# Kernel tuning notes

Hardware: AMD Instinct MI355X
Metric: run time of the kernel (lower is better)

The kernel has to match this reference:

```python
import jax, jax.numpy as jnp
import numpy as np

KEEP_P = 0.75  # 1 - dropout_p, dropout_p = 0.25

def setup_inputs() -> dict:
    key = jax.random.key(0)
    k1, k2, k3, k4 = jax.random.split(key, 4)
    B, Sq, Skv, D, Dv = 8, 2048, 2048, 128, 128
    x1 = jax.random.normal(k1, (B, Sq, D), dtype=jnp.float32)
    x2 = jax.random.normal(k2, (B, Skv, D), dtype=jnp.float32)
    x3 = jax.random.normal(k3, (B, Skv, Dv), dtype=jnp.float32)
    # torch Dropout(p): mask = bernoulli(keep_p) / keep_p
    keep = jax.random.bernoulli(k4, KEEP_P, (B, Sq, Skv))
    dropout_mask = keep.astype(jnp.float32) / KEEP_P
    return {"x1": x1, "x2": x2, "x3": x3, "dropout_mask": dropout_mask}

def reference(x1, x2, x3, dropout_mask):
    # scores: [B, Sq, Skv] = x1 @ x2^T (no scale: scale_factor is None)
    scores = jnp.einsum("bqd,bkd->bqk", x1, x2)
    probs = jax.nn.softmax(scores, axis=-1)
    probs = probs * dropout_mask  # dropout with fixed mask
    out = jnp.einsum("bqk,bkv->bqv", probs, x3)  # [B, Sq, Dv]
    return out
```

## Files before the change

### kernel.cpp

```cpp
#include <hip/hip_runtime.h>
#include <stdint.h>

#define SQ 2048
#define SKV 2048
#define DD 128
#define NB 8
#define LOG2E 1.44269504088896340736f
#define M0L 57.70780163555852f

typedef float    f4v __attribute__((ext_vector_type(4)));
typedef __bf16   bf8 __attribute__((ext_vector_type(8)));
typedef _Float16 h8  __attribute__((ext_vector_type(8)));

__device__ __forceinline__ void async16(const void* g, void* l) {
    __builtin_amdgcn_global_load_lds(
        (const __attribute__((address_space(1))) void*)g,
        (__attribute__((address_space(3))) void*)l, 16, 0, 0);
}

__global__ void preprocess(const float* __restrict__ x2, _Float16* __restrict__ Kh,
                           const float* __restrict__ x3, __bf16* __restrict__ VTf) {
    __shared__ __bf16 tile[32][33];
    const int bid = blockIdx.x;
    if (bid < 1024) {
        int tid = bid * 256 + threadIdx.x;
        int d8 = tid & 15;
        int kv = (tid >> 4) & (SKV - 1);
        int b  = tid >> 15;
        const float* p = x2 + ((size_t)b * SKV + kv) * DD + d8 * 8;
        f4v a0 = *(const f4v*)p;
        f4v a1 = *(const f4v*)(p + 4);
        h8 h;
#pragma unroll
        for (int c = 0; c < 4; c++) {
            h[c]     = (_Float16)a0[c];
            h[c + 4] = (_Float16)a1[c];
        }
        int s = d8 >> 2, g = d8 & 3, kb32 = kv >> 5, row = kv & 31;
        int h8idx = s * 128 + ((row >> 4) << 6) + g * 16 + (row & 15);
        *(h8*)(Kh + (size_t)(b * 64 + kb32) * 4096 + (size_t)h8idx * 8) = h;
    } else {
        int t = bid - 1024;
        int kb32 = t & 63, dv0 = ((t >> 6) & 3) * 32, b = t >> 8;
        int tx = threadIdx.x & 31, ty = threadIdx.x >> 5;
        const float* src = x3 + ((size_t)b * SKV + kb32 * 32 + ty) * DD + dv0 + tx;
#pragma unroll
        for (int i = 0; i < 32; i += 8)
            tile[ty + i][tx] = (__bf16)src[(size_t)i * DD];
        __syncthreads();
        int pcol = (tx < 16) ? ((tx >> 2) << 3) + (tx & 3)
                             : (((tx - 16) >> 2) << 3) + 4 + (tx & 3);
        __bf16* base = VTf + (size_t)(b * 64 + kb32) * 4096
                     + ((pcol >> 3) << 7) + (pcol & 7);
#pragma unroll
        for (int i = 0; i < 32; i += 8) {
            int dv = dv0 + ty + i;
            base[((dv >> 4) << 9) + ((dv & 15) << 3)] = tile[tx][ty + i];
        }
    }
}

__global__ __launch_bounds__(256, 1) void attn_kernel(
    const float* __restrict__ Qf, const _Float16* __restrict__ Kh,
    const __bf16* __restrict__ Vt, const float* __restrict__ mask,
    float* __restrict__ out) {
    __shared__ __align__(16) char smem[3][16384];
    const int lin = blockIdx.x;
    const int b = lin & 7;
    const int qblk = lin >> 3;
    const int tid = threadIdx.x;
    const int w = tid >> 6, lane = tid & 63;
    const int g = lane >> 4, n = lane & 15;
    const int qb = qblk * 64 + w * 16;
    const int niter = SKV / 32;

    const _Float16* Kt0 = Kh + (size_t)b * 64 * 4096;
    const __bf16*   Vt0 = Vt + (size_t)b * 64 * 4096;
    auto stageTo = [&](char* buf, int it) {
#pragma unroll
        for (int jj = 0; jj < 4; jj++) {
            int j = w * 4 + jj;
            if (j < 8)
                async16(Kt0 + (size_t)it * 4096 + j * 512 + lane * 8,
                        (void*)(buf + j * 1024));
            else
                async16(Vt0 + (size_t)it * 4096 + (j - 8) * 512 + lane * 8,
                        (void*)(buf + 8192 + (j - 8) * 1024));
        }
    };

    const float* Qrow = Qf + ((size_t)b * SQ + qb + n) * DD + g * 8;
    h8 qf[4];
#pragma unroll
    for (int s = 0; s < 4; s++) {
        f4v v0 = *(const f4v*)(Qrow + s * 32);
        f4v v1 = *(const f4v*)(Qrow + s * 32 + 4);
#pragma unroll
        for (int c = 0; c < 4; c++) {
            qf[s][c]     = (_Float16)v0[c];
            qf[s][c + 4] = (_Float16)v1[c];
        }
    }

    const float* mrow = mask + ((size_t)b * SQ + qb + n) * SKV;

    const f4v zero = {0.f, 0.f, 0.f, 0.f};
    f4v o_acc[8];
#pragma unroll
    for (int t = 0; t < 8; t++) o_acc[t] = zero;
    float l_run = 0.f;

    char* s0p = &smem[0][0];
    char* s1p = &smem[1][0];
    char* s2p = &smem[2][0];

    stageTo(s0p, 0);
    asm volatile("" ::: "memory");
    f4v mA0 = *(const f4v*)(mrow + g * 4);
    f4v mA1 = *(const f4v*)(mrow + 16 + g * 4);
    asm volatile("" ::: "memory");
    stageTo(s1p, 1);
    asm volatile("" ::: "memory");
    f4v mB0 = *(const f4v*)(mrow + 32 + g * 4);
    f4v mB1 = *(const f4v*)(mrow + 48 + g * 4);
    f4v mC0 = zero, mC1 = zero;

    auto body = [&](int it, const char* bufR, char* bufW,
                    const f4v& u0, const f4v& u1, f4v& t0, f4v& t1) {
        asm volatile("s_waitcnt vmcnt(6)" ::: "memory");
        __builtin_amdgcn_s_barrier();
        asm volatile("" ::: "memory");
        const int itp = (it + 2 < niter) ? it + 2 : niter - 1;
        stageTo(bufW, itp);
        t0 = *(const f4v*)(mrow + itp * 32 + g * 4);
        t1 = *(const f4v*)(mrow + itp * 32 + 16 + g * 4);

        const _Float16* Lk = (const _Float16*)bufR;
        const __bf16*   Lv = (const __bf16*)(bufR + 8192);

        f4v sa0 = zero, sa1 = zero;
#pragma unroll
        for (int s = 0; s < 4; s++) {
            h8 a0 = *(const h8*)(Lk + (size_t)(s * 128 + g * 16 + n) * 8);
            h8 a1 = *(const h8*)(Lk + (size_t)(s * 128 + 64 + g * 16 + n) * 8);
            sa0 = __builtin_amdgcn_mfma_f32_16x16x32_f16(a0, qf[s], sa0, 0, 0, 0);
            sa1 = __builtin_amdgcn_mfma_f32_16x16x32_f16(a1, qf[s], sa1, 0, 0, 0);
        }

        bf8 pf;
#pragma unroll
        for (int r = 0; r < 4; r++) {
            float e0 = exp2f(sa0[r] * LOG2E - M0L);
            float e1 = exp2f(sa1[r] * LOG2E - M0L);
            l_run += e0 + e1;
            pf[r]     = (__bf16)(e0 * u0[r]);
            pf[r + 4] = (__bf16)(e1 * u1[r]);
        }

#pragma unroll
        for (int t = 0; t < 8; t++) {
            bf8 vf = *(const bf8*)(Lv + (size_t)(t * 64 + g * 16 + n) * 8);
            o_acc[t] = __builtin_amdgcn_mfma_f32_16x16x32_bf16(pf, vf, o_acc[t], 0, 0, 0);
        }
    };

    for (int it = 0; it < niter; it += 3) {
        body(it,     s0p, s2p, mA0, mA1, mC0, mC1);
        if (it + 1 < niter)
            body(it + 1, s1p, s0p, mB0, mB1, mA0, mA1);
        if (it + 2 < niter)
            body(it + 2, s2p, s1p, mC0, mC1, mB0, mB1);
    }

    l_run += __shfl_xor(l_run, 16);
    l_run += __shfl_xor(l_run, 32);
    float sc[4];
#pragma unroll
    for (int r = 0; r < 4; r++)
        sc[r] = 1.0f / __shfl(l_run, g * 4 + r);
    float* orow = out + ((size_t)b * SQ + qb + g * 4) * DD + n;
#pragma unroll
    for (int t = 0; t < 8; t++)
#pragma unroll
        for (int r = 0; r < 4; r++)
            orow[(size_t)r * DD + t * 16] = o_acc[t][r] * sc[r];
}

extern "C" void kernel_launch(void* const* d_in, const int* in_sizes, int n_in,
                              void* d_out, int out_size, void* d_ws, size_t ws_size,
                              hipStream_t stream) {
    const float* x1   = (const float*)d_in[0];
    const float* x2   = (const float*)d_in[1];
    const float* x3   = (const float*)d_in[2];
    const float* mask = (const float*)d_in[3];
    float* out = (float*)d_out;

    const size_t kelems = (size_t)NB * SKV * DD;
    _Float16* Kh  = (_Float16*)d_ws;
    __bf16*   VTf = (__bf16*)(Kh + kelems);

    hipLaunchKernelGGL(preprocess, dim3(3072), dim3(256), 0, stream,
                       x2, Kh, x3, VTf);
    hipLaunchKernelGGL(attn_kernel, dim3(256), dim3(256), 0, stream,
                       x1, Kh, VTf, mask, out);
}
```

Baseline: 253.4 us.

## Split KV range across two waves per block and drop LDS staging

The attention kernel now runs 128-thread blocks covering 16 query rows each, with the two waves splitting the key range in halves. K and V fragments are loaded directly from global memory into registers with one-iteration prefetch, replacing the triple-buffered LDS pipeline and its barriers. Partial outputs and row sums are combined through shared memory at the end. This gives four times as many blocks and more resident waves per CU to hide latency, at the cost of more redundant K/V reads from L2 and an extra reduction step.

```diff
diff --git a/kernel.cpp b/kernel.cpp
--- a/kernel.cpp
+++ b/kernel.cpp
@@ -7,16 +7,11 @@
 #define NB 8
 #define LOG2E 1.44269504088896340736f
 #define M0L 57.70780163555852f
+#define KEEP_INV 1.3333333333333333f
 
 typedef float    f4v __attribute__((ext_vector_type(4)));
 typedef __bf16   bf8 __attribute__((ext_vector_type(8)));
 typedef _Float16 h8  __attribute__((ext_vector_type(8)));
-
-__device__ __forceinline__ void async16(const void* g, void* l) {
-    __builtin_amdgcn_global_load_lds(
-        (const __attribute__((address_space(1))) void*)g,
-        (__attribute__((address_space(3))) void*)l, 16, 0, 0);
-}
 
 __global__ void preprocess(const float* __restrict__ x2, _Float16* __restrict__ Kh,
                            const float* __restrict__ x3, __bf16* __restrict__ VTf) {
@@ -60,34 +55,21 @@
     }
 }
 
-__global__ __launch_bounds__(256, 1) void attn_kernel(
+__global__ __launch_bounds__(128, 2) void attn_kernel(
     const float* __restrict__ Qf, const _Float16* __restrict__ Kh,
     const __bf16* __restrict__ Vt, const float* __restrict__ mask,
     float* __restrict__ out) {
-    __shared__ __align__(16) char smem[3][16384];
+    __shared__ float redO[2][2048];
+    __shared__ float redL[2][16];
     const int lin = blockIdx.x;
     const int b = lin & 7;
     const int qblk = lin >> 3;
     const int tid = threadIdx.x;
     const int w = tid >> 6, lane = tid & 63;
     const int g = lane >> 4, n = lane & 15;
-    const int qb = qblk * 64 + w * 16;
-    const int niter = SKV / 32;
-
-    const _Float16* Kt0 = Kh + (size_t)b * 64 * 4096;
-    const __bf16*   Vt0 = Vt + (size_t)b * 64 * 4096;
-    auto stageTo = [&](char* buf, int it) {
-#pragma unroll
-        for (int jj = 0; jj < 4; jj++) {
-            int j = w * 4 + jj;
-            if (j < 8)
-                async16(Kt0 + (size_t)it * 4096 + j * 512 + lane * 8,
-                        (void*)(buf + j * 1024));
-            else
-                async16(Vt0 + (size_t)it * 4096 + (j - 8) * 512 + lane * 8,
-                        (void*)(buf + 8192 + (j - 8) * 1024));
-        }
-    };
+    const int qb = qblk * 16;
+    const int kb0 = w * 32;
+    const int niter = 32;
 
     const float* Qrow = Qf + ((size_t)b * SQ + qb + n) * DD + g * 8;
     h8 qf[4];
@@ -102,7 +84,24 @@
         }
     }
 
-    const float* mrow = mask + ((size_t)b * SQ + qb + n) * SKV;
+    const _Float16* Kt0 = Kh + (size_t)(b * 64 + kb0) * 4096;
+    const __bf16*   Vt0 = Vt + (size_t)(b * 64 + kb0) * 4096;
+    const float*    mrow = mask + ((size_t)b * SQ + qb + n) * SKV + w * 1024;
+
+    h8  Ka[8];
+    bf8 Va[8];
+#pragma unroll
+    for (int s = 0; s < 4; s++) {
+        Ka[s * 2]     = *(const h8*)(Kt0 + (size_t)(s * 128 + g * 16 + n) * 8);
+        Ka[s * 2 + 1] = *(const h8*)(Kt0 + (size_t)(s * 128 + 64 + g * 16 + n) * 8);
+    }
+#pragma unroll
+    for (int t = 0; t < 8; t++)
+        Va[t] = *(const bf8*)(Vt0 + (size_t)(t * 64 + g * 16 + n) * 8);
+    f4v c0 = *(const f4v*)(mrow + g * 4);
+    f4v c1 = *(const f4v*)(mrow + 16 + g * 4);
+    f4v p0 = *(const f4v*)(mrow + 32 + g * 4);
+    f4v p1 = *(const f4v*)(mrow + 48 + g * 4);
 
     const f4v zero = {0.f, 0.f, 0.f, 0.f};
     f4v o_acc[8];
@@ -110,41 +109,20 @@
     for (int t = 0; t < 8; t++) o_acc[t] = zero;
     float l_run = 0.f;
 
-    char* s0p = &smem[0][0];
-    char* s1p = &smem[1][0];
-    char* s2p = &smem[2][0];
-
-    stageTo(s0p, 0);
-    asm volatile("" ::: "memory");
-    f4v mA0 = *(const f4v*)(mrow + g * 4);
-    f4v mA1 = *(const f4v*)(mrow + 16 + g * 4);
-    asm volatile("" ::: "memory");
-    stageTo(s1p, 1);
-    asm volatile("" ::: "memory");
-    f4v mB0 = *(const f4v*)(mrow + 32 + g * 4);
-    f4v mB1 = *(const f4v*)(mrow + 48 + g * 4);
-    f4v mC0 = zero, mC1 = zero;
-
-    auto body = [&](int it, const char* bufR, char* bufW,
-                    const f4v& u0, const f4v& u1, f4v& t0, f4v& t1) {
-        asm volatile("s_waitcnt vmcnt(6)" ::: "memory");
-        __builtin_amdgcn_s_barrier();
-        asm volatile("" ::: "memory");
-        const int itp = (it + 2 < niter) ? it + 2 : niter - 1;
-        stageTo(bufW, itp);
-        t0 = *(const f4v*)(mrow + itp * 32 + g * 4);
-        t1 = *(const f4v*)(mrow + itp * 32 + 16 + g * 4);
-
-        const _Float16* Lk = (const _Float16*)bufR;
-        const __bf16*   Lv = (const __bf16*)(bufR + 8192);
+    for (int it = 0; it < niter; it++) {
+        const int itn = (it + 1 < niter) ? it + 1 : it;
 
         f4v sa0 = zero, sa1 = zero;
 #pragma unroll
         for (int s = 0; s < 4; s++) {
-            h8 a0 = *(const h8*)(Lk + (size_t)(s * 128 + g * 16 + n) * 8);
-            h8 a1 = *(const h8*)(Lk + (size_t)(s * 128 + 64 + g * 16 + n) * 8);
-            sa0 = __builtin_amdgcn_mfma_f32_16x16x32_f16(a0, qf[s], sa0, 0, 0, 0);
-            sa1 = __builtin_amdgcn_mfma_f32_16x16x32_f16(a1, qf[s], sa1, 0, 0, 0);
+            sa0 = __builtin_amdgcn_mfma_f32_16x16x32_f16(Ka[s * 2],     qf[s], sa0, 0, 0, 0);
+            sa1 = __builtin_amdgcn_mfma_f32_16x16x32_f16(Ka[s * 2 + 1], qf[s], sa1, 0, 0, 0);
+        }
+        const _Float16* Kn = Kt0 + (size_t)itn * 4096;
+#pragma unroll
+        for (int s = 0; s < 4; s++) {
+            Ka[s * 2]     = *(const h8*)(Kn + (size_t)(s * 128 + g * 16 + n) * 8);
+            Ka[s * 2 + 1] = *(const h8*)(Kn + (size_t)(s * 128 + 64 + g * 16 + n) * 8);
         }
 
         bf8 pf;
@@ -153,37 +131,44 @@
             float e0 = exp2f(sa0[r] * LOG2E - M0L);
             float e1 = exp2f(sa1[r] * LOG2E - M0L);
             l_run += e0 + e1;
-            pf[r]     = (__bf16)(e0 * u0[r]);
-            pf[r + 4] = (__bf16)(e1 * u1[r]);
+            pf[r]     = (__bf16)(e0 * c0[r]);
+            pf[r + 4] = (__bf16)(e1 * c1[r]);
         }
 
 #pragma unroll
-        for (int t = 0; t < 8; t++) {
-            bf8 vf = *(const bf8*)(Lv + (size_t)(t * 64 + g * 16 + n) * 8);
-            o_acc[t] = __builtin_amdgcn_mfma_f32_16x16x32_bf16(pf, vf, o_acc[t], 0, 0, 0);
-        }
-    };
+        for (int t = 0; t < 8; t++)
+            o_acc[t] = __builtin_amdgcn_mfma_f32_16x16x32_bf16(pf, Va[t], o_acc[t], 0, 0, 0);
+        const __bf16* Vn = Vt0 + (size_t)itn * 4096;
+#pragma unroll
+        for (int t = 0; t < 8; t++)
+            Va[t] = *(const bf8*)(Vn + (size_t)(t * 64 + g * 16 + n) * 8);
 
-    for (int it = 0; it < niter; it += 3) {
-        body(it,     s0p, s2p, mA0, mA1, mC0, mC1);
-        if (it + 1 < niter)
-            body(it + 1, s1p, s0p, mB0, mB1, mA0, mA1);
-        if (it + 2 < niter)
-            body(it + 2, s2p, s1p, mC0, mC1, mB0, mB1);
+        c0 = p0; c1 = p1;
+        const int it2 = (it + 2 < niter) ? it + 2 : niter - 1;
+        p0 = *(const f4v*)(mrow + it2 * 32 + g * 4);
+        p1 = *(const f4v*)(mrow + it2 * 32 + 16 + g * 4);
     }
 
     l_run += __shfl_xor(l_run, 16);
     l_run += __shfl_xor(l_run, 32);
-    float sc[4];
-#pragma unroll
-    for (int r = 0; r < 4; r++)
-        sc[r] = 1.0f / __shfl(l_run, g * 4 + r);
-    float* orow = out + ((size_t)b * SQ + qb + g * 4) * DD + n;
 #pragma unroll
     for (int t = 0; t < 8; t++)
 #pragma unroll
         for (int r = 0; r < 4; r++)
-            orow[(size_t)r * DD + t * 16] = o_acc[t][r] * sc[r];
+            redO[w][(g * 4 + r) * 128 + t * 16 + n] = o_acc[t][r];
+    if (g == 0) redL[w][n] = l_run;
+    __syncthreads();
+
+    const int row = tid >> 3;
+    const int c16 = (tid & 7) * 16;
+    float scale = 1.0f / (redL[0][row] + redL[1][row]);
+    float* o = out + ((size_t)b * SQ + qb + row) * DD + c16;
+#pragma unroll
+    for (int v = 0; v < 4; v++) {
+        f4v a = *(const f4v*)&redO[0][row * 128 + c16 + v * 4]
+              + *(const f4v*)&redO[1][row * 128 + c16 + v * 4];
+        *(f4v*)(o + v * 4) = a * scale;
+    }
 }
 
 extern "C" void kernel_launch(void* const* d_in, const int* in_sizes, int n_in,
@@ -201,6 +186,6 @@
 
     hipLaunchKernelGGL(preprocess, dim3(3072), dim3(256), 0, stream,
                        x2, Kh, x3, VTf);
-    hipLaunchKernelGGL(attn_kernel, dim3(256), dim3(256), 0, stream,
+    hipLaunchKernelGGL(attn_kernel, dim3(NB * 128), dim3(128), 0, stream,
                        x1, Kh, VTf, mask, out);
 }
```

New measurement: 272.0 us. 7.4% more time.
